# Optimization experiments

Hardware: AMD Instinct MI355X
Metric: run time of the kernel (lower is better)

## Reference

```python
import jax, jax.numpy as jnp
import numpy as np

N = 50000      # nodes
E = 800000     # edges (before self-loops)
IN_C = 128
HID = 64
HEADS = 4
OUT_C = 64
NEG_SLOPE = 0.2  # PyG GATConv default


def setup_inputs() -> dict:
    key = jax.random.key(0)
    ks = jax.random.split(key, 12)
    def glorot(k, shape, fan):
        return jax.random.normal(k, shape, jnp.float32) * (1.0 / np.sqrt(fan))
    return {
        "x": jax.random.normal(ks[0], (N, IN_C), jnp.float32),
        "edge_index": jax.random.randint(ks[1], (2, E), 0, N, dtype=jnp.int32),
        # layer 1: in -> heads*hid, concat=True
        "W1": glorot(ks[2], (IN_C, HEADS * HID), IN_C),
        "att1_src": glorot(ks[3], (HEADS, HID), HID),
        "att1_dst": glorot(ks[4], (HEADS, HID), HID),
        "b1": jnp.zeros((HEADS * HID,), jnp.float32),
        # layer 2: heads*hid -> out, heads=1
        "W2": glorot(ks[5], (HEADS * HID, OUT_C), HEADS * HID),
        "att2_src": glorot(ks[6], (1, OUT_C), OUT_C),
        "att2_dst": glorot(ks[7], (1, OUT_C), OUT_C),
        "b2": jnp.zeros((OUT_C,), jnp.float32),
    }


def gat_conv(x, src, dst, W, a_src, a_dst, b, heads):
    """One PyG-style GATConv (self-loops already included in src/dst)."""
    n = x.shape[0]
    c = W.shape[1] // heads
    h = (x @ W).reshape(n, heads, c)                    # [N,H,C]
    alpha_s = jnp.sum(h * a_src, axis=-1)               # [N,H]
    alpha_d = jnp.sum(h * a_dst, axis=-1)               # [N,H]
    e = jax.nn.leaky_relu(alpha_s[src] + alpha_d[dst], NEG_SLOPE)  # [E',H]
    # segment softmax over incoming edges of each destination node
    m = jax.ops.segment_max(e, dst, num_segments=n)
    m = jnp.where(jnp.isfinite(m), m, 0.0)
    ex = jnp.exp(e - m[dst])
    denom = jax.ops.segment_sum(ex, dst, num_segments=n)
    alpha = ex / (denom[dst] + 1e-16)                   # [E',H]
    msg = h[src] * alpha[..., None]                     # [E',H,C]
    out = jax.ops.segment_sum(msg, dst, num_segments=n) # [N,H,C]
    return out.reshape(n, heads * c) + b


def reference(x, edge_index, W1, att1_src, att1_dst, b1, W2, att2_src, att2_dst, b2):
    n = x.shape[0]
    loop = jnp.arange(n, dtype=edge_index.dtype)
    src = jnp.concatenate([edge_index[0], loop])
    dst = jnp.concatenate([edge_index[1], loop])
    # dropout is identity in eval mode
    h = gat_conv(x, src, dst, W1, att1_src, att1_dst, b1, HEADS)
    h = jax.nn.elu(h)
    return gat_conv(h, src, dst, W2, att2_src, att2_dst, b2, 1)
```

## Files before the change

### kernel.cpp

```cpp
#include <hip/hip_runtime.h>
#include <hip/hip_bf16.h>
#include <hip/hip_fp16.h>

#define NNODES 50000
#define NEDGES 800000
#define EPLUS  (NEDGES + NNODES)
#define EHALF  (EPLUS / 2)
#define INC    128
#define HID    64
#define NHEADS 4
#define OUTC   64
#define NEG_SLOPE 0.2f
#define STRIDE 48
#define NSLOTS (NNODES * STRIDE)

typedef __attribute__((ext_vector_type(8))) short short8;
typedef __attribute__((ext_vector_type(4))) float floatx4;
typedef __attribute__((ext_vector_type(2))) float floatx2;

#define BF2LO(u) __uint_as_float((u) << 16)
#define BF2HI(u) __uint_as_float((u) & 0xffff0000u)

__global__ void k_uvec(const float* __restrict__ W1, const float* __restrict__ a1s,
                       const float* __restrict__ a1d, float* __restrict__ us,
                       float* __restrict__ ud) {
    int i = threadIdx.x + blockIdx.x * blockDim.x;
    if (i >= NHEADS * INC) return;
    int h = i >> 7, k = i & 127;
    const float* wp = W1 + (size_t)k * (NHEADS * HID) + h * HID;
    const float* sp = a1s + h * HID;
    const float* dp = a1d + h * HID;
    float s = 0.f, d = 0.f;
#pragma unroll 8
    for (int c = 0; c < HID; c++) { float w = wp[c]; s += w * sp[c]; d += w * dp[c]; }
    us[i] = s; ud[i] = d;
}

__global__ void k_prep_x(const float* __restrict__ x, const float* __restrict__ us,
                         const float* __restrict__ ud, __hip_bfloat16* __restrict__ xb,
                         float* __restrict__ as1, float* __restrict__ ad1,
                         int* __restrict__ cursor) {
    int w = threadIdx.x >> 6;
    int lane = threadIdx.x & 63;
    int n = blockIdx.x * 4 + w;
    if (n >= NNODES) return;
    float2 xv = *(const float2*)(x + (size_t)n * INC + lane * 2);
    __hip_bfloat16 o[2];
    o[0] = __float2bfloat16(xv.x);
    o[1] = __float2bfloat16(xv.y);
    *(unsigned*)(xb + (size_t)n * INC + lane * 2) = *(unsigned*)o;
    float ps[4], pd[4];
#pragma unroll
    for (int h = 0; h < 4; h++) {
        float2 sv = *(const float2*)(us + h * INC + lane * 2);
        float2 dv = *(const float2*)(ud + h * INC + lane * 2);
        ps[h] = xv.x * sv.x + xv.y * sv.y;
        pd[h] = xv.x * dv.x + xv.y * dv.y;
    }
#pragma unroll
    for (int off = 1; off < 64; off <<= 1) {
#pragma unroll
        for (int h = 0; h < 4; h++) {
            ps[h] += __shfl_xor(ps[h], off, 64);
            pd[h] += __shfl_xor(pd[h], off, 64);
        }
    }
    if (lane == 0) {
        float4 vs = {ps[0], ps[1], ps[2], ps[3]};
        float4 vd = {pd[0], pd[1], pd[2], pd[3]};
        *(float4*)&as1[n * 4] = vs;
        *(float4*)&ad1[n * 4] = vd;
        cursor[n] = 0;
    }
}

__global__ void k_scat_w1(const int* __restrict__ ei, int* __restrict__ cursor,
                          int* __restrict__ recs) {
    int e = blockIdx.x * blockDim.x + threadIdx.x;
    if (e >= EHALF) return;
    int eB = e + EHALF;
    int srcA, dstA;
    if (e < NEDGES) { srcA = ei[e]; dstA = ei[NEDGES + e]; }
    else            { srcA = dstA = e - NEDGES; }
    int srcB, dstB;
    if (eB < NEDGES) { srcB = ei[eB]; dstB = ei[NEDGES + eB]; }
    else             { srcB = dstB = eB - NEDGES; }
    int slotA = atomicAdd(&cursor[dstA], 1);
    int slotB = atomicAdd(&cursor[dstB], 1);
    if (slotA < STRIDE) recs[dstA * STRIDE + slotA] = srcA;
    if (slotB < STRIDE) recs[dstB * STRIDE + slotB] = srcB;
}

__global__ void k_agg1n(const __hip_bfloat16* __restrict__ xb, const int* __restrict__ cnt,
                        const int* __restrict__ recs, const float* __restrict__ as1,
                        const float* __restrict__ ad1, __hip_bfloat16* __restrict__ aggb) {
    int w = threadIdx.x >> 6;
    int lane = threadIdx.x & 63;
    int half = lane >> 5;
    int lh = lane & 31;
    int n = blockIdx.x * 4 + w;
    if (n >= NNODES) return;
    int deg = cnt[n]; if (deg > STRIDE) deg = STRIDE;
    int beg = n * STRIDE, end = beg + deg;
    float4 adv = *(const float4*)&ad1[n * 4];

    const unsigned* xp = (const unsigned*)xb;
    unsigned choff = (unsigned)lh * 2u;

    floatx2 a00 = {0.f,0.f}, a01 = {0.f,0.f};
    floatx2 a10 = {0.f,0.f}, a11 = {0.f,0.f};
    floatx2 a20 = {0.f,0.f}, a21 = {0.f,0.f};
    floatx2 a30 = {0.f,0.f}, a31 = {0.f,0.f};
    floatx2 d01 = {0.f,0.f}, d23 = {0.f,0.f};

    int jj = beg;
    for (; jj + 3 < end; jj += 4) {
        int2 ss = *(const int2*)(recs + jj + 2 * half);
        int sA = ss.x, sB = ss.y;
        float4 svA = *(const float4*)&as1[sA * 4];
        float4 svB = *(const float4*)&as1[sB * 4];
        unsigned oA = (unsigned)sA * 64u + choff;
        unsigned oB = (unsigned)sB * 64u + choff;
        uint2 uA = *(const uint2*)(xp + oA);
        uint2 uB = *(const uint2*)(xp + oB);
        float t;
        t = svA.x + adv.x; t = (t > 0.f) ? t : NEG_SLOPE * t; float wA0 = __expf(t);
        t = svA.y + adv.y; t = (t > 0.f) ? t : NEG_SLOPE * t; float wA1 = __expf(t);
        t = svA.z + adv.z; t = (t > 0.f) ? t : NEG_SLOPE * t; float wA2 = __expf(t);
        t = svA.w + adv.w; t = (t > 0.f) ? t : NEG_SLOPE * t; float wA3 = __expf(t);
        t = svB.x + adv.x; t = (t > 0.f) ? t : NEG_SLOPE * t; float wB0 = __expf(t);
        t = svB.y + adv.y; t = (t > 0.f) ? t : NEG_SLOPE * t; float wB1 = __expf(t);
        t = svB.z + adv.z; t = (t > 0.f) ? t : NEG_SLOPE * t; float wB2 = __expf(t);
        t = svB.w + adv.w; t = (t > 0.f) ? t : NEG_SLOPE * t; float wB3 = __expf(t);
        d01 += (floatx2){wA0, wA1} + (floatx2){wB0, wB1};
        d23 += (floatx2){wA2, wA3} + (floatx2){wB2, wB3};
        floatx2 xA01 = {BF2LO(uA.x), BF2HI(uA.x)};
        floatx2 xA23 = {BF2LO(uA.y), BF2HI(uA.y)};
        floatx2 xB01 = {BF2LO(uB.x), BF2HI(uB.x)};
        floatx2 xB23 = {BF2LO(uB.y), BF2HI(uB.y)};
        a00 += (floatx2){wA0, wA0} * xA01;  a01 += (floatx2){wA0, wA0} * xA23;
        a10 += (floatx2){wA1, wA1} * xA01;  a11 += (floatx2){wA1, wA1} * xA23;
        a20 += (floatx2){wA2, wA2} * xA01;  a21 += (floatx2){wA2, wA2} * xA23;
        a30 += (floatx2){wA3, wA3} * xA01;  a31 += (floatx2){wA3, wA3} * xA23;
        a00 += (floatx2){wB0, wB0} * xB01;  a01 += (floatx2){wB0, wB0} * xB23;
        a10 += (floatx2){wB1, wB1} * xB01;  a11 += (floatx2){wB1, wB1} * xB23;
        a20 += (floatx2){wB2, wB2} * xB01;  a21 += (floatx2){wB2, wB2} * xB23;
        a30 += (floatx2){wB3, wB3} * xB01;  a31 += (floatx2){wB3, wB3} * xB23;
    }
    for (; jj < end; jj += 2) {
        int idx = jj + half;
        bool v = idx < end;
        int s = recs[v ? idx : beg];
        float4 sv = *(const float4*)&as1[s * 4];
        float t;
        t = sv.x + adv.x; t = (t > 0.f) ? t : NEG_SLOPE * t; float e0 = __expf(t);
        t = sv.y + adv.y; t = (t > 0.f) ? t : NEG_SLOPE * t; float e1 = __expf(t);
        t = sv.z + adv.z; t = (t > 0.f) ? t : NEG_SLOPE * t; float e2 = __expf(t);
        t = sv.w + adv.w; t = (t > 0.f) ? t : NEG_SLOPE * t; float e3 = __expf(t);
        float w0 = v ? e0 : 0.f, w1 = v ? e1 : 0.f;
        float w2 = v ? e2 : 0.f, w3 = v ? e3 : 0.f;
        d01 += (floatx2){w0, w1};
        d23 += (floatx2){w2, w3};
        unsigned o = (unsigned)s * 64u + choff;
        uint2 u = *(const uint2*)(xp + o);
        floatx2 x01 = {BF2LO(u.x), BF2HI(u.x)};
        floatx2 x23 = {BF2LO(u.y), BF2HI(u.y)};
        a00 += (floatx2){w0, w0} * x01;  a01 += (floatx2){w0, w0} * x23;
        a10 += (floatx2){w1, w1} * x01;  a11 += (floatx2){w1, w1} * x23;
        a20 += (floatx2){w2, w2} * x01;  a21 += (floatx2){w2, w2} * x23;
        a30 += (floatx2){w3, w3} * x01;  a31 += (floatx2){w3, w3} * x23;
    }

#define XSUM2(vv) { vv.x += __shfl_xor(vv.x, 32, 64); vv.y += __shfl_xor(vv.y, 32, 64); }
    XSUM2(a00) XSUM2(a01) XSUM2(a10) XSUM2(a11)
    XSUM2(a20) XSUM2(a21) XSUM2(a30) XSUM2(a31)
    XSUM2(d01) XSUM2(d23)
#undef XSUM2

    float dA = half ? d23.x : d01.x;
    float dB = half ? d23.y : d01.y;
    float iA = 1.f / (dA + 1e-16f);
    float iB = 1.f / (dB + 1e-16f);
    floatx2 sa = half ? a20 : a00;
    floatx2 sb = half ? a21 : a01;
    floatx2 sc = half ? a30 : a10;
    floatx2 sd = half ? a31 : a11;
    __hip_bfloat16 o4[4];
    unsigned long long pk;
    size_t base = ((size_t)n * 4 + half * 2) * INC + lh * 4;
    o4[0] = __float2bfloat16(sa.x * iA); o4[1] = __float2bfloat16(sa.y * iA);
    o4[2] = __float2bfloat16(sb.x * iA); o4[3] = __float2bfloat16(sb.y * iA);
    __builtin_memcpy(&pk, o4, 8);
    __builtin_nontemporal_store(pk, (unsigned long long*)(aggb + base));
    o4[0] = __float2bfloat16(sc.x * iB); o4[1] = __float2bfloat16(sc.y * iB);
    o4[2] = __float2bfloat16(sd.x * iB); o4[3] = __float2bfloat16(sd.y * iB);
    __builtin_memcpy(&pk, o4, 8);
    __builtin_nontemporal_store(pk, (unsigned long long*)(aggb + base + INC));
}

__global__ void k_swz12(const float* __restrict__ W1, const float* __restrict__ W2,
                        __hip_bfloat16* __restrict__ Bsw1, __hip_bfloat16* __restrict__ Bsw2) {
    int i = blockIdx.x * blockDim.x + threadIdx.x;
    if (blockIdx.y == 0) {
        if (i >= 4 * 4 * 4 * 64 * 8) return;
        int j = i & 7, l = (i >> 3) & 63, t = (i >> 9) & 3, s = (i >> 11) & 3, h = i >> 13;
        int k = s * 32 + (l >> 4) * 8 + j;
        int col = h * 64 + t * 16 + (l & 15);
        Bsw1[i] = __float2bfloat16(W1[(size_t)k * 256 + col]);
    } else {
        if (i >= 8 * 4 * 64 * 8) return;
        int j = i & 7, l = (i >> 3) & 63, t = (i >> 9) & 3, s = i >> 11;
        int k = s * 32 + (l >> 4) * 8 + j;
        int col = t * 16 + (l & 15);
        Bsw2[i] = __float2bfloat16(W2[(size_t)k * 64 + col]);
    }
}

__global__ void k_mm1(const __hip_bfloat16* __restrict__ A,
                      const __hip_bfloat16* __restrict__ Bsw,
                      const float* __restrict__ b1,
                      __hip_bfloat16* __restrict__ out1b) {
    int row0 = blockIdx.x * 64;
    int h = blockIdx.y;
    int w = threadIdx.x >> 6;
    int l = threadIdx.x & 63;
    int lg = l >> 4, lm = l & 15;
    int ra = row0 + w * 16 + lm;
    if (ra >= NNODES) ra = NNODES - 1;

    floatx4 acc[4];
#pragma unroll
    for (int t = 0; t < 4; t++) acc[t] = (floatx4){0.f, 0.f, 0.f, 0.f};

    const __hip_bfloat16* ap = A + ((size_t)ra * NHEADS + h) * INC + lg * 8;
#pragma unroll
    for (int s = 0; s < 4; s++) {
        short8 a = *(const short8*)(ap + s * 32);
#pragma unroll
        for (int t = 0; t < 4; t++) {
            short8 b = *(const short8*)(Bsw + (((h * 4 + s) * 4 + t) * 64 + l) * 8);
            acc[t] = __builtin_amdgcn_mfma_f32_16x16x32_bf16(a, b, acc[t], 0, 0, 0);
        }
    }
#pragma unroll
    for (int t = 0; t < 4; t++) {
        int col = h * 64 + t * 16 + lm;
        float bias = b1[col];
#pragma unroll
        for (int r = 0; r < 4; r++) {
            int row = row0 + w * 16 + lg * 4 + r;
            if (row < NNODES) {
                float v = acc[t][r] + bias;
                v = (v > 0.f) ? v : (__expf(v) - 1.f);
                out1b[(size_t)row * 256 + col] = __float2bfloat16(v);
            }
        }
    }
}

__global__ void k_mm2(const __hip_bfloat16* __restrict__ A,
                      const __hip_bfloat16* __restrict__ Bsw,
                      const float* __restrict__ a2s, const float* __restrict__ a2d,
                      __hip_bfloat16* __restrict__ h2b,
                      float* __restrict__ as2, float* __restrict__ ad2) {
    int row0 = blockIdx.x * 64;
    int w = threadIdx.x >> 6;
    int l = threadIdx.x & 63;
    int lg = l >> 4, lm = l & 15;
    int ra = row0 + w * 16 + lm;
    if (ra >= NNODES) ra = NNODES - 1;

    floatx4 acc[4];
#pragma unroll
    for (int t = 0; t < 4; t++) acc[t] = (floatx4){0.f, 0.f, 0.f, 0.f};

    const __hip_bfloat16* ap = A + (size_t)ra * 256 + lg * 8;
#pragma unroll
    for (int s = 0; s < 8; s++) {
        short8 a = *(const short8*)(ap + s * 32);
#pragma unroll
        for (int t = 0; t < 4; t++) {
            short8 b = *(const short8*)(Bsw + ((s * 4 + t) * 64 + l) * 8);
            acc[t] = __builtin_amdgcn_mfma_f32_16x16x32_bf16(a, b, acc[t], 0, 0, 0);
        }
    }
    float ps[4] = {0.f, 0.f, 0.f, 0.f};
    float pd[4] = {0.f, 0.f, 0.f, 0.f};
#pragma unroll
    for (int t = 0; t < 4; t++) {
        int col = t * 16 + lm;
        float vs = a2s[col], vd = a2d[col];
#pragma unroll
        for (int r = 0; r < 4; r++) {
            int row = row0 + w * 16 + lg * 4 + r;
            float v = acc[t][r];
            if (row < NNODES) h2b[(size_t)row * OUTC + col] = __float2bfloat16(v);
            ps[r] += v * vs;
            pd[r] += v * vd;
        }
    }
#pragma unroll
    for (int off = 1; off < 16; off <<= 1) {
#pragma unroll
        for (int r = 0; r < 4; r++) {
            ps[r] += __shfl_xor(ps[r], off, 64);
            pd[r] += __shfl_xor(pd[r], off, 64);
        }
    }
    if (lm == 0) {
#pragma unroll
        for (int r = 0; r < 4; r++) {
            int row = row0 + w * 16 + lg * 4 + r;
            if (row < NNODES) { as2[row] = ps[r]; ad2[row] = pd[r]; }
        }
    }
}

__global__ void k_agg2n(const __hip_bfloat16* __restrict__ h2b, const int* __restrict__ cnt,
                        const int* __restrict__ recs, const float* __restrict__ as2,
                        const float* __restrict__ ad2, const float* __restrict__ b2,
                        float* __restrict__ out) {
    int w = threadIdx.x >> 6;
    int lane = threadIdx.x & 63;
    int half = lane >> 5;
    int lh = lane & 31;
    int n = blockIdx.x * 4 + w;
    if (n >= NNODES) return;
    int deg = cnt[n]; if (deg > STRIDE) deg = STRIDE;
    int beg = n * STRIDE, end = beg + deg;
    float adv = ad2[n];
    const unsigned* hp = (const unsigned*)h2b;

    floatx2 acc = {0.f, 0.f};
    float den = 0.f;

    int jj = beg;
    for (; jj + 3 < end; jj += 4) {
        int2 ss = *(const int2*)(recs + jj + 2 * half);
        int sA = ss.x, sB = ss.y;
        float tA = as2[sA] + adv;
        float tB = as2[sB] + adv;
        unsigned gA = hp[(unsigned)sA * 32u + lh];
        unsigned gB = hp[(unsigned)sB * 32u + lh];
        tA = (tA > 0.f) ? tA : NEG_SLOPE * tA; float wA = __expf(tA);
        tB = (tB > 0.f) ? tB : NEG_SLOPE * tB; float wB = __expf(tB);
        acc += (floatx2){wA, wA} * (floatx2){BF2LO(gA), BF2HI(gA)};
        acc += (floatx2){wB, wB} * (floatx2){BF2LO(gB), BF2HI(gB)};
        den += wA + wB;
    }
    for (; jj < end; jj += 2) {
        int idx = jj + half;
        bool v = idx < end;
        int s = recs[v ? idx : beg];
        float t = as2[s] + adv;
        t = (t > 0.f) ? t : NEG_SLOPE * t;
        float wv = v ? __expf(t) : 0.f;
        unsigned g = hp[(unsigned)s * 32u + lh];
        acc += (floatx2){wv, wv} * (floatx2){BF2LO(g), BF2HI(g)};
        den += wv;
    }
    acc.x += __shfl_xor(acc.x, 32, 64);
    acc.y += __shfl_xor(acc.y, 32, 64);
    den   += __shfl_xor(den,   32, 64);
    if (half == 0) {
        float inv = 1.f / (den + 1e-16f);
        float2 bb = *(const float2*)(b2 + lh * 2);
        float2 ov;
        ov.x = acc.x * inv + bb.x;
        ov.y = acc.y * inv + bb.y;
        unsigned long long pk;
        __builtin_memcpy(&pk, &ov, 8);
        __builtin_nontemporal_store(pk, (unsigned long long*)(out + (size_t)n * OUTC + lh * 2));
    }
}

extern "C" void kernel_launch(void* const* d_in, const int* in_sizes, int n_in,
                              void* d_out, int out_size, void* d_ws, size_t ws_size,
                              hipStream_t stream) {
    const float* x   = (const float*)d_in[0];
    const int*   ei  = (const int*)d_in[1];
    const float* W1  = (const float*)d_in[2];
    const float* a1s = (const float*)d_in[3];
    const float* a1d = (const float*)d_in[4];
    const float* b1  = (const float*)d_in[5];
    const float* W2  = (const float*)d_in[6];
    const float* a2s = (const float*)d_in[7];
    const float* a2d = (const float*)d_in[8];
    const float* b2  = (const float*)d_in[9];
    float* out = (float*)d_out;

    char* p = (char*)d_ws;
    auto carve = [&](size_t bytes) -> void* {
        void* r = (void*)p;
        p += (bytes + 255) & ~(size_t)255;
        return r;
    };
    __hip_bfloat16* xb    = (__hip_bfloat16*)carve((size_t)NNODES * INC * 2);
    __hip_bfloat16* aggb  = (__hip_bfloat16*)carve((size_t)NNODES * NHEADS * INC * 2);
    __hip_bfloat16* out1b = (__hip_bfloat16*)carve((size_t)NNODES * 256 * 2);
    __hip_bfloat16* h2b   = (__hip_bfloat16*)carve((size_t)NNODES * OUTC * 2);
    __hip_bfloat16* Bsw1  = (__hip_bfloat16*)carve((size_t)4 * 4 * 4 * 64 * 8 * 2);
    __hip_bfloat16* Bsw2  = (__hip_bfloat16*)carve((size_t)8 * 4 * 64 * 8 * 2);
    float* us      = (float*)carve((size_t)NHEADS * INC * 4);
    float* ud      = (float*)carve((size_t)NHEADS * INC * 4);
    float* as1     = (float*)carve((size_t)NNODES * NHEADS * 4);
    float* ad1     = (float*)carve((size_t)NNODES * NHEADS * 4);
    float* as2     = (float*)carve((size_t)NNODES * 4);
    float* ad2     = (float*)carve((size_t)NNODES * 4);
    int*   cursor  = (int*)carve((size_t)NNODES * 4);
    int*   recs    = (int*)carve((size_t)NSLOTS * 4);

    k_uvec<<<2, 256, 0, stream>>>(W1, a1s, a1d, us, ud);
    k_prep_x<<<(NNODES + 3) / 4, 256, 0, stream>>>(x, us, ud, xb, as1, ad1, cursor);
    dim3 gsw(128, 2);
    k_swz12<<<gsw, 256, 0, stream>>>(W1, W2, Bsw1, Bsw2);

    k_scat_w1<<<(EHALF + 255) / 256, 256, 0, stream>>>(ei, cursor, recs);

    k_agg1n<<<(NNODES + 3) / 4, 256, 0, stream>>>(xb, cursor, recs, as1, ad1, aggb);
    dim3 g1((NNODES + 63) / 64, NHEADS);
    k_mm1<<<g1, 256, 0, stream>>>(aggb, Bsw1, b1, out1b);

    k_mm2<<<(NNODES + 63) / 64, 256, 0, stream>>>(out1b, Bsw2, a2s, a2d, h2b, as2, ad2);
    k_agg2n<<<(NNODES + 3) / 4, 256, 0, stream>>>(h2b, cursor, recs, as2, ad2, b2, out);
}
```

Before: 293.8 us.

## Precompute fp16 edge attention weights during scatter and bucket nodes across XCDs

The edge scatter kernel now computes each edge's four exp(leaky_relu) attention weights and stores them packed as fp16 next to the source index. The layer-1 aggregation then reads these weights instead of gathering as1 and recomputing exponentials. Work is also split into eight destination-node buckets keyed on blockIdx&7, so each XCD's L2 handles a contiguous node range. To do this, each scatter block rereads the whole edge list and filters for its own bucket. The costs are eight-fold reads of edge_index, an extra 8-byte-per-slot weight array, and reduced weight precision from fp16.

```diff
diff --git a/kernel.cpp b/kernel.cpp
--- a/kernel.cpp
+++ b/kernel.cpp
@@ -5,7 +5,8 @@
 #define NNODES 50000
 #define NEDGES 800000
 #define EPLUS  (NEDGES + NNODES)
-#define EHALF  (EPLUS / 2)
+#define NB8    (NNODES / 8)
+#define SCHUNKS ((EPLUS + 511) / 512)
 #define INC    128
 #define HID    64
 #define NHEADS 4
@@ -75,34 +76,56 @@
 }
 
 __global__ void k_scat_w1(const int* __restrict__ ei, int* __restrict__ cursor,
-                          int* __restrict__ recs) {
-    int e = blockIdx.x * blockDim.x + threadIdx.x;
-    if (e >= EHALF) return;
-    int eB = e + EHALF;
-    int srcA, dstA;
-    if (e < NEDGES) { srcA = ei[e]; dstA = ei[NEDGES + e]; }
-    else            { srcA = dstA = e - NEDGES; }
-    int srcB, dstB;
-    if (eB < NEDGES) { srcB = ei[eB]; dstB = ei[NEDGES + eB]; }
-    else             { srcB = dstB = eB - NEDGES; }
-    int slotA = atomicAdd(&cursor[dstA], 1);
-    int slotB = atomicAdd(&cursor[dstB], 1);
-    if (slotA < STRIDE) recs[dstA * STRIDE + slotA] = srcA;
-    if (slotB < STRIDE) recs[dstB * STRIDE + slotB] = srcB;
+                          const float* __restrict__ as, const float* __restrict__ ad,
+                          int* __restrict__ recs, uint2* __restrict__ recw) {
+    int chunk = blockIdx.x >> 3;
+    int bucket = blockIdx.x & 7;
+    int lo = bucket * NB8, hi = lo + NB8;
+    int e0 = chunk * 512 + threadIdx.x;
+#pragma unroll
+    for (int q = 0; q < 2; q++) {
+        int e = e0 + q * 256;
+        if (e >= EPLUS) break;
+        int src, dst;
+        if (e < NEDGES) {
+            src = __builtin_nontemporal_load(ei + e);
+            dst = __builtin_nontemporal_load(ei + NEDGES + e);
+        } else {
+            src = dst = e - NEDGES;
+        }
+        if (dst < lo || dst >= hi) continue;
+        int slot = atomicAdd(&cursor[dst], 1);
+        if (slot >= STRIDE) continue;
+        float4 sv = *(const float4*)&as[src * 4];
+        float4 dv = *(const float4*)&ad[dst * 4];
+        float t, w0, w1, w2, w3;
+        t = sv.x + dv.x; t = (t > 0.f) ? t : NEG_SLOPE * t; w0 = __expf(t);
+        t = sv.y + dv.y; t = (t > 0.f) ? t : NEG_SLOPE * t; w1 = __expf(t);
+        t = sv.z + dv.z; t = (t > 0.f) ? t : NEG_SLOPE * t; w2 = __expf(t);
+        t = sv.w + dv.w; t = (t > 0.f) ? t : NEG_SLOPE * t; w3 = __expf(t);
+        __half2 p01 = __floats2half2_rn(w0, w1);
+        __half2 p23 = __floats2half2_rn(w2, w3);
+        int idx = dst * STRIDE + slot;
+        recs[idx] = src;
+        uint2 wp;
+        wp.x = *(unsigned*)&p01; wp.y = *(unsigned*)&p23;
+        recw[idx] = wp;
+    }
 }
 
 __global__ void k_agg1n(const __hip_bfloat16* __restrict__ xb, const int* __restrict__ cnt,
-                        const int* __restrict__ recs, const float* __restrict__ as1,
-                        const float* __restrict__ ad1, __hip_bfloat16* __restrict__ aggb) {
+                        const int* __restrict__ recs, const uint2* __restrict__ recw,
+                        __hip_bfloat16* __restrict__ aggb) {
     int w = threadIdx.x >> 6;
     int lane = threadIdx.x & 63;
     int half = lane >> 5;
     int lh = lane & 31;
-    int n = blockIdx.x * 4 + w;
-    if (n >= NNODES) return;
+    int bucket = blockIdx.x & 7;
+    int local = (blockIdx.x >> 3) * 4 + w;
+    if (local >= NB8) return;
+    int n = bucket * NB8 + local;
     int deg = cnt[n]; if (deg > STRIDE) deg = STRIDE;
     int beg = n * STRIDE, end = beg + deg;
-    float4 adv = *(const float4*)&ad1[n * 4];
 
     const unsigned* xp = (const unsigned*)xb;
     unsigned choff = (unsigned)lh * 2u;
@@ -117,21 +140,18 @@
     for (; jj + 3 < end; jj += 4) {
         int2 ss = *(const int2*)(recs + jj + 2 * half);
         int sA = ss.x, sB = ss.y;
-        float4 svA = *(const float4*)&as1[sA * 4];
-        float4 svB = *(const float4*)&as1[sB * 4];
+        uint2 wAu = recw[jj + 2 * half];
+        uint2 wBu = recw[jj + 2 * half + 1];
         unsigned oA = (unsigned)sA * 64u + choff;
         unsigned oB = (unsigned)sB * 64u + choff;
         uint2 uA = *(const uint2*)(xp + oA);
         uint2 uB = *(const uint2*)(xp + oB);
-        float t;
-        t = svA.x + adv.x; t = (t > 0.f) ? t : NEG_SLOPE * t; float wA0 = __expf(t);
-        t = svA.y + adv.y; t = (t > 0.f) ? t : NEG_SLOPE * t; float wA1 = __expf(t);
-        t = svA.z + adv.z; t = (t > 0.f) ? t : NEG_SLOPE * t; float wA2 = __expf(t);
-        t = svA.w + adv.w; t = (t > 0.f) ? t : NEG_SLOPE * t; float wA3 = __expf(t);
-        t = svB.x + adv.x; t = (t > 0.f) ? t : NEG_SLOPE * t; float wB0 = __expf(t);
-        t = svB.y + adv.y; t = (t > 0.f) ? t : NEG_SLOPE * t; float wB1 = __expf(t);
-        t = svB.z + adv.z; t = (t > 0.f) ? t : NEG_SLOPE * t; float wB2 = __expf(t);
-        t = svB.w + adv.w; t = (t > 0.f) ? t : NEG_SLOPE * t; float wB3 = __expf(t);
+        __half2 A01 = *(__half2*)&wAu.x, A23 = *(__half2*)&wAu.y;
+        __half2 B01 = *(__half2*)&wBu.x, B23 = *(__half2*)&wBu.y;
+        float wA0 = __low2float(A01), wA1 = __high2float(A01);
+        float wA2 = __low2float(A23), wA3 = __high2float(A23);
+        float wB0 = __low2float(B01), wB1 = __high2float(B01);
+        float wB2 = __low2float(B23), wB3 = __high2float(B23);
         d01 += (floatx2){wA0, wA1} + (floatx2){wB0, wB1};
         d23 += (floatx2){wA2, wA3} + (floatx2){wB2, wB3};
         floatx2 xA01 = {BF2LO(uA.x), BF2HI(uA.x)};
@@ -151,14 +171,13 @@
         int idx = jj + half;
         bool v = idx < end;
         int s = recs[v ? idx : beg];
-        float4 sv = *(const float4*)&as1[s * 4];
-        float t;
-        t = sv.x + adv.x; t = (t > 0.f) ? t : NEG_SLOPE * t; float e0 = __expf(t);
-        t = sv.y + adv.y; t = (t > 0.f) ? t : NEG_SLOPE * t; float e1 = __expf(t);
-        t = sv.z + adv.z; t = (t > 0.f) ? t : NEG_SLOPE * t; float e2 = __expf(t);
-        t = sv.w + adv.w; t = (t > 0.f) ? t : NEG_SLOPE * t; float e3 = __expf(t);
-        float w0 = v ? e0 : 0.f, w1 = v ? e1 : 0.f;
-        float w2 = v ? e2 : 0.f, w3 = v ? e3 : 0.f;
+        uint2 wu = recw[v ? idx : beg];
+        unsigned w01i = v ? wu.x : 0u;
+        unsigned w23i = v ? wu.y : 0u;
+        __half2 p01 = *(__half2*)&w01i;
+        __half2 p23 = *(__half2*)&w23i;
+        float w0 = __low2float(p01), w1 = __high2float(p01);
+        float w2 = __low2float(p23), w3 = __high2float(p23);
         d01 += (floatx2){w0, w1};
         d23 += (floatx2){w2, w3};
         unsigned o = (unsigned)s * 64u + choff;
@@ -324,8 +343,10 @@
     int lane = threadIdx.x & 63;
     int half = lane >> 5;
     int lh = lane & 31;
-    int n = blockIdx.x * 4 + w;
-    if (n >= NNODES) return;
+    int bucket = blockIdx.x & 7;
+    int local = (blockIdx.x >> 3) * 4 + w;
+    if (local >= NB8) return;
+    int n = bucket * NB8 + local;
     int deg = cnt[n]; if (deg > STRIDE) deg = STRIDE;
     int beg = n * STRIDE, end = beg + deg;
     float adv = ad2[n];
@@ -409,18 +430,19 @@
     float* ad2     = (float*)carve((size_t)NNODES * 4);
     int*   cursor  = (int*)carve((size_t)NNODES * 4);
     int*   recs    = (int*)carve((size_t)NSLOTS * 4);
+    uint2* recw    = (uint2*)carve((size_t)NSLOTS * 8);
 
     k_uvec<<<2, 256, 0, stream>>>(W1, a1s, a1d, us, ud);
     k_prep_x<<<(NNODES + 3) / 4, 256, 0, stream>>>(x, us, ud, xb, as1, ad1, cursor);
     dim3 gsw(128, 2);
     k_swz12<<<gsw, 256, 0, stream>>>(W1, W2, Bsw1, Bsw2);
 
-    k_scat_w1<<<(EHALF + 255) / 256, 256, 0, stream>>>(ei, cursor, recs);
-
-    k_agg1n<<<(NNODES + 3) / 4, 256, 0, stream>>>(xb, cursor, recs, as1, ad1, aggb);
+    k_scat_w1<<<SCHUNKS * 8, 256, 0, stream>>>(ei, cursor, as1, ad1, recs, recw);
+
+    k_agg1n<<<1563 * 8, 256, 0, stream>>>(xb, cursor, recs, recw, aggb);
     dim3 g1((NNODES + 63) / 64, NHEADS);
     k_mm1<<<g1, 256, 0, stream>>>(aggb, Bsw1, b1, out1b);
 
     k_mm2<<<(NNODES + 63) / 64, 256, 0, stream>>>(out1b, Bsw2, a2s, a2d, h2b, as2, ad2);
-    k_agg2n<<<(NNODES + 3) / 4, 256, 0, stream>>>(h2b, cursor, recs, as2, ad2, b2, out);
-}
+    k_agg2n<<<1563 * 8, 256, 0, stream>>>(h2b, cursor, recs, as2, ad2, b2, out);
+}
```

After: 297.5 us. Within noise of the previous version (+1.3%).
